# Kernel optimization log

Measured on AMD Instinct MI355X. Metric: run time of the kernel, lower is better.

Reference implementation:

```python
import jax, jax.numpy as jnp
import numpy as np

NUM_EMB = 1024
EMB_DIM = 256
BETA = 0.25


def setup_inputs() -> dict:
    key = jax.random.key(0)
    k1, k2 = jax.random.split(key)
    z = jax.random.normal(k1, (64, 32, 32, EMB_DIM), dtype=jnp.float32)
    # RandomUniform(-1/N, 1/N) init, shape (embedding_dimension, number_embeddings)
    embeddings = jax.random.uniform(
        k2, (EMB_DIM, NUM_EMB), dtype=jnp.float32,
        minval=-1.0 / NUM_EMB, maxval=1.0 / NUM_EMB)
    return {"z": z, "embeddings": embeddings}


def reference(z, embeddings):
    beta = BETA
    z_flat = z.reshape(-1, EMB_DIM)                      # [N, D]
    # squared L2 distances via ||z||^2 + ||e||^2 - 2 z @ e
    distances = (jnp.sum(z_flat ** 2, axis=1, keepdims=True)
                 + jnp.sum(embeddings ** 2, axis=0)
                 - 2.0 * (z_flat @ embeddings))          # [N, K]
    encoding_indices = jnp.argmin(distances, axis=1)     # [N] int
    quantized = embeddings.T[encoding_indices].reshape(z.shape)  # gather rows of e^T
    vq_loss = jnp.mean((quantized - jax.lax.stop_gradient(z)) ** 2)
    commitment_loss = beta * jnp.mean((jax.lax.stop_gradient(quantized) - z) ** 2)
    quantized_st = z + jax.lax.stop_gradient(quantized - z)  # straight-through
    # perplexity from codebook usage histogram
    counts = jnp.zeros((NUM_EMB,), dtype=distances.dtype).at[encoding_indices].add(1.0)
    avg_probs = counts / encoding_indices.shape[0]
    perplexity = jnp.exp(-jnp.sum(avg_probs * jnp.log(avg_probs + 1e-10)))
    return (quantized_st, encoding_indices, vq_loss, commitment_loss, perplexity)
```

## Files before the change

kernel.cpp:

```cpp
#include <hip/hip_runtime.h>
#include <math.h>

#define NUM_EMB 1024
#define EMB_DIM 256
#define NROWS   65536
#define NTHREADS 256
#define MTHREADS 1024
#define EPSF 1.5e-3f
#define GCAP 458752
#define LLCAP 3837

#define OFF_IDX  16777216
#define OFF_VQ   16842752

#define WS_C2    0
#define WS_HIST  4096
#define WS_LOSS  8192
#define WS_GCNT  8196
#define WS_R2    8448
#define WS_SLOT  270592
#define WS_ETF   794880
#define WS_ETB   1843456
#define WS_RMIN  2367744
#define WS_GLIST 2629888

typedef __attribute__((ext_vector_type(8))) short bf16x8;
typedef __attribute__((ext_vector_type(4))) float f32x4;

#define BAR_LGKM() do {                                        \
    asm volatile("s_waitcnt lgkmcnt(0)" ::: "memory");         \
    __builtin_amdgcn_s_barrier();                              \
    asm volatile("" ::: "memory");                             \
  } while (0)

__device__ __forceinline__ unsigned short f2bf(float x) {
  unsigned u = __float_as_uint(x);
  unsigned r = (u + 0x7FFFu + ((u >> 16) & 1u)) >> 16;
  return (unsigned short)r;
}

__global__ __launch_bounds__(NTHREADS) void vq_pt(
    const float* __restrict__ emb, float* __restrict__ cvec,
    int* __restrict__ hist, float* __restrict__ loss, int* __restrict__ gcnt,
    float* __restrict__ embTf, unsigned short* __restrict__ embTbf) {
  __shared__ float t[64][65];
  const int tid = threadIdx.x;
  if (blockIdx.x < 4) {
    int k = blockIdx.x * NTHREADS + tid;
    float s = 0.f;
    for (int d = 0; d < EMB_DIM; ++d) {
      float v = emb[d * NUM_EMB + k];
      s = __fadd_rn(s, __fmul_rn(v, v));
    }
    cvec[k] = s;
    hist[k] = 0;
    if (k == 0) { *loss = 0.f; *gcnt = 0; }
  } else {
    const int b = blockIdx.x - 4;
    const int kt = b & 15, dt = b >> 4;
    #pragma unroll
    for (int it = 0; it < 16; ++it) {
      int i = tid + it * NTHREADS, r = i >> 6, c = i & 63;
      t[r][c] = emb[(dt * 64 + r) * NUM_EMB + kt * 64 + c];
    }
    __syncthreads();
    #pragma unroll
    for (int it = 0; it < 16; ++it) {
      int i = tid + it * NTHREADS, r = i >> 6, c = i & 63;
      float v = t[c][r];
      embTf[(kt * 64 + r) * EMB_DIM + dt * 64 + c] = v;
      embTbf[(kt * 64 + r) * EMB_DIM + dt * 64 + c] = f2bf(v);
    }
  }
}

__global__ __launch_bounds__(NTHREADS) void vq_r2k(
    const float* __restrict__ z, float* __restrict__ r2out) {
  __shared__ float zc[64][36];
  __shared__ float pmm[64][2][4];
  const int tid = threadIdx.x;
  const int n0 = blockIdx.x * 64;
  const float* zrow = z + (size_t)n0 * EMB_DIM;
  const int prow = tid >> 2, pm = tid & 3;
  float racc[2][2] = {{0.f, 0.f}, {0.f, 0.f}};
  for (int dc = 0; dc < 8; ++dc) {
    __syncthreads();
    #pragma unroll
    for (int it = 0; it < 2; ++it) {
      int i = tid + it * NTHREADS, row = i >> 3, f4 = i & 7;
      *(float4*)(&zc[row][f4 * 4]) = *(const float4*)(zrow + row * EMB_DIM + dc * 32 + f4 * 4);
    }
    __syncthreads();
    const int half = dc >> 2;
    #pragma unroll
    for (int q = 0; q < 4; ++q)
      #pragma unroll
      for (int jj = 0; jj < 2; ++jj) {
        float v = zc[prow][(pm * 2 + jj) + 8 * q];
        racc[half][jj] = __fadd_rn(racc[half][jj], __fmul_rn(v, v));
      }
  }
  pmm[prow][0][pm] = __fadd_rn(racc[0][0], racc[0][1]);
  pmm[prow][1][pm] = __fadd_rn(racc[1][0], racc[1][1]);
  __syncthreads();
  if (tid < 64) {
    float h0 = __fadd_rn(__fadd_rn(pmm[tid][0][0], pmm[tid][0][1]),
                         __fadd_rn(pmm[tid][0][2], pmm[tid][0][3]));
    float h1 = __fadd_rn(__fadd_rn(pmm[tid][1][0], pmm[tid][1][1]),
                         __fadd_rn(pmm[tid][1][2], pmm[tid][1][3]));
    r2out[n0 + tid] = __fadd_rn(h0, h1);
  }
}

__global__ __launch_bounds__(MTHREADS, 4) void vq_mfma(
    const float* __restrict__ z, const unsigned short* __restrict__ embTbf,
    const float* __restrict__ cvec, unsigned long long* __restrict__ slots,
    int* __restrict__ gcnt, unsigned int* __restrict__ glist,
    int* __restrict__ grm) {
  __shared__ unsigned short zc[256][256];
  __shared__ unsigned short Bl[2][8192];

  int* caps = (int*)&Bl[1][0];
  unsigned int* llist = (unsigned int*)caps + 259;

  const int tid = threadIdx.x;
  const int lane = tid & 63, wave = tid >> 6;
  const int quad = lane >> 4, l15 = lane & 15;
  const int rg = wave >> 2, cg = wave & 3;
  const int n0 = blockIdx.x * 256;

  if (tid < 256) {
    grm[n0 + tid] = 0x7F000000;
    slots[n0 + tid] = ~0ULL;
  }

  #pragma unroll
  for (int it = 0; it < 8; ++it) {
    int g = tid + it * MTHREADS, row = g >> 5, u = g & 31;
    const float* src = z + (size_t)(n0 + row) * EMB_DIM + u * 8;
    float4 a = *(const float4*)src;
    float4 b = *(const float4*)(src + 4);
    uint4 w;
    w.x = ((unsigned)f2bf(a.y) << 16) | f2bf(a.x);
    w.y = ((unsigned)f2bf(a.w) << 16) | f2bf(a.z);
    w.z = ((unsigned)f2bf(b.y) << 16) | f2bf(b.x);
    w.w = ((unsigned)f2bf(b.w) << 16) | f2bf(b.z);
    *(uint4*)(&zc[row][(u ^ (row & 7)) * 8]) = w;
  }

  const int bn = tid >> 2, bseg = tid & 3;
  const size_t bofs = (size_t)bn * EMB_DIM + (size_t)bseg * 8;
  const int bunit = bn * 4 + (bseg ^ ((bn >> 1) & 3));
  int bidx[4];
  #pragma unroll
  for (int ct = 0; ct < 4; ++ct) {
    int cn = cg * 64 + ct * 16 + l15;
    bidx[ct] = (cn * 4 + (quad ^ ((cn >> 1) & 3))) * 8;
  }

  uint4 p0 = *(const uint4*)(embTbf + bofs);
  BAR_LGKM();
  *(uint4*)(&Bl[0][(size_t)bunit * 8]) = p0;
  uint4 bpre = *(const uint4*)(embTbf + 32 + bofs);
  BAR_LGKM();

  for (int j = 0; j < 4; ++j) {
    f32x4 acc[4][4];
    #pragma unroll
    for (int rt = 0; rt < 4; ++rt)
      #pragma unroll
      for (int ct = 0; ct < 4; ++ct)
        acc[rt][ct] = (f32x4){0.f, 0.f, 0.f, 0.f};
    float c2r[4];
    #pragma unroll
    for (int ct = 0; ct < 4; ++ct)
      c2r[ct] = cvec[j * 256 + cg * 64 + ct * 16 + l15] + 1.0f;

    for (int kc = 0; kc < 8; ++kc) {
      const int c = j * 8 + kc;
      if (c < 31)
        *(uint4*)(&Bl[(c + 1) & 1][(size_t)bunit * 8]) = bpre;
      if (c + 2 < 32)
        bpre = *(const uint4*)(embTbf + (size_t)((c + 2) >> 3) * 65536 +
                               (size_t)((c + 2) & 7) * 32 + bofs);
      bf16x8 av[4], bv[4];
      #pragma unroll
      for (int rt = 0; rt < 4; ++rt) {
        int row = rg * 64 + rt * 16 + l15;
        av[rt] = *(const bf16x8*)(&zc[row][((kc * 4 + quad) ^ (l15 & 7)) * 8]);
      }
      #pragma unroll
      for (int ct = 0; ct < 4; ++ct)
        bv[ct] = *(const bf16x8*)(&Bl[c & 1][(size_t)bidx[ct]]);
      #pragma unroll
      for (int rt = 0; rt < 4; ++rt)
        #pragma unroll
        for (int ct = 0; ct < 4; ++ct)
          acc[rt][ct] = __builtin_amdgcn_mfma_f32_16x16x32_bf16(av[rt], bv[ct], acc[rt][ct], 0, 0, 0);
      BAR_LGKM();
    }
    if (tid < 256) caps[tid] = 0x7F000000;
    if (tid == 0) caps[256] = 0;
    BAR_LGKM();

    #pragma unroll
    for (int rt = 0; rt < 4; ++rt)
      #pragma unroll
      for (int reg = 0; reg < 4; ++reg) {
        float m = 1e30f;
        #pragma unroll
        for (int ct = 0; ct < 4; ++ct) {
          float d = fmaf(-2.f, acc[rt][ct][reg], c2r[ct]);
          m = fminf(m, d);
        }
        #pragma unroll
        for (int off = 1; off < 16; off <<= 1)
          m = fminf(m, __shfl_xor(m, off));
        if (l15 == 0)
          atomicMin(&caps[rg * 64 + rt * 16 + quad * 4 + reg], __float_as_int(m));
      }
    BAR_LGKM();

    if (tid < 256) {
      int lm = caps[tid];
      int old = atomicMin(&grm[n0 + tid], lm);
      caps[tid] = lm < old ? lm : old;
    }
    BAR_LGKM();

    #pragma unroll
    for (int rt = 0; rt < 4; ++rt)
      #pragma unroll
      for (int reg = 0; reg < 4; ++reg) {
        int rowl = rg * 64 + rt * 16 + quad * 4 + reg;
        float fmin = __int_as_float(caps[rowl]);
        #pragma unroll
        for (int ct = 0; ct < 4; ++ct) {
          float d = fmaf(-2.f, acc[rt][ct][reg], c2r[ct]);
          bool pred = (d <= fmin + EPSF);
          unsigned long long msk = __ballot(pred);
          if (msk) {
            int leader = (int)(__ffsll((long long)msk) - 1);
            int cnt = (int)__popcll(msk);
            int base0 = 0;
            if (lane == leader) base0 = atomicAdd(&caps[256], cnt);
            base0 = __shfl(base0, leader);
            if (pred) {
              int id = base0 + (int)__popcll(msk & ((1ULL << lane) - 1ULL));
              int k = j * 256 + cg * 64 + ct * 16 + l15;
              if (id < LLCAP)
                llist[id] = ((unsigned)(n0 + rowl) << 10) | (unsigned)k;
            }
          }
        }
      }
    BAR_LGKM();
    if (tid == 0) {
      int c = caps[256]; if (c > LLCAP) c = LLCAP;
      caps[258] = c;
      caps[257] = atomicAdd(gcnt, c);
    }
    BAR_LGKM();
    {
      int cnt = caps[258], base = caps[257];
      for (int i = tid; i < cnt; i += MTHREADS)
        if (base + i < GCAP) glist[base + i] = llist[i];
    }
    BAR_LGKM();
  }
}

__global__ __launch_bounds__(NTHREADS) void vq_refine(
    const float* __restrict__ z, const float* __restrict__ embTf,
    const float* __restrict__ r2, const float* __restrict__ cvec,
    const int* __restrict__ gcnt, const unsigned int* __restrict__ glist,
    unsigned long long* __restrict__ slots) {
  int n = *gcnt; if (n > GCAP) n = GCAP;
  for (int i = blockIdx.x * NTHREADS + threadIdx.x; i < n;
       i += gridDim.x * NTHREADS) {
    unsigned e = glist[i];
    int grow = (int)(e >> 10), k = (int)(e & 1023);
    const float* zr = z + (size_t)grow * EMB_DIM;
    const float* er = embTf + (size_t)k * EMB_DIM;
    float s = 0.f;
    for (int d = 0; d < EMB_DIM; ++d)
      s = fmaf(zr[d], er[d], s);
    float dist = __fsub_rn(__fadd_rn(r2[grow], cvec[k]), __fmul_rn(2.0f, s));
    unsigned long long key =
        ((unsigned long long)__float_as_uint(dist) << 32) | (unsigned)k;
    atomicMin(&slots[grow], key);
  }
}

__global__ __launch_bounds__(NTHREADS) void vq_epi(
    const float* __restrict__ z, const float* __restrict__ embTf,
    const unsigned long long* __restrict__ slots,
    float* __restrict__ out, int* __restrict__ hist, float* __restrict__ loss) {
  __shared__ int ks[64];
  __shared__ float wsum[4];
  const int tid = threadIdx.x;
  const int n0 = blockIdx.x * 64;
  const float* zrow = z + (size_t)n0 * EMB_DIM;
  if (tid < 64) {
    int k = (int)(slots[n0 + tid] & 1023ULL);
    ks[tid] = k;
    out[OFF_IDX + n0 + tid] = (float)k;
    atomicAdd(&hist[k], 1);
  }
  __syncthreads();
  float sumsq = 0.f;
  #pragma unroll
  for (int it = 0; it < 16; ++it) {
    int g = tid + it * NTHREADS;
    int row = g >> 6;
    int d = (g & 63) * 4;
    int k = ks[row];
    float4 zv = *(const float4*)(zrow + row * EMB_DIM + d);
    float4 q = *(const float4*)(embTf + (size_t)k * EMB_DIM + d);
    float4 df;
    df.x = q.x - zv.x; df.y = q.y - zv.y; df.z = q.z - zv.z; df.w = q.w - zv.w;
    sumsq = fmaf(df.x, df.x, sumsq);
    sumsq = fmaf(df.y, df.y, sumsq);
    sumsq = fmaf(df.z, df.z, sumsq);
    sumsq = fmaf(df.w, df.w, sumsq);
    *(float4*)(out + (size_t)(n0 + row) * EMB_DIM + d) = q;
  }
  #pragma unroll
  for (int off = 32; off > 0; off >>= 1) sumsq += __shfl_down(sumsq, off);
  if ((tid & 63) == 0) wsum[tid >> 6] = sumsq;
  __syncthreads();
  if (tid == 0) atomicAdd(loss, wsum[0] + wsum[1] + wsum[2] + wsum[3]);
}

__global__ __launch_bounds__(NTHREADS) void vq_finalize(
    const int* __restrict__ hist, const float* __restrict__ loss,
    float* __restrict__ out) {
  __shared__ float ws[4];
  int tid = threadIdx.x;
  float s = 0.f;
  for (int k = tid; k < NUM_EMB; k += NTHREADS) {
    float p = (float)hist[k] * (1.0f / 65536.0f);
    s += p * logf(p + 1e-10f);
  }
  #pragma unroll
  for (int off = 32; off > 0; off >>= 1) s += __shfl_down(s, off);
  if ((tid & 63) == 0) ws[tid >> 6] = s;
  __syncthreads();
  if (tid == 0) {
    float tot = ws[0] + ws[1] + ws[2] + ws[3];
    float vq = *loss * (1.0f / 16777216.0f);
    out[OFF_VQ + 0] = vq;
    out[OFF_VQ + 1] = 0.25f * vq;
    out[OFF_VQ + 2] = expf(-tot);
  }
}

extern "C" void kernel_launch(void* const* d_in, const int* in_sizes, int n_in,
                              void* d_out, int out_size, void* d_ws, size_t ws_size,
                              hipStream_t stream) {
  const float* z   = (const float*)d_in[0];
  const float* emb = (const float*)d_in[1];
  float* out = (float*)d_out;
  char* ws = (char*)d_ws;
  float* cvec   = (float*)(ws + WS_C2);
  int*   hist   = (int*)(ws + WS_HIST);
  float* loss   = (float*)(ws + WS_LOSS);
  int*   gcnt   = (int*)(ws + WS_GCNT);
  float* r2     = (float*)(ws + WS_R2);
  unsigned long long* slots = (unsigned long long*)(ws + WS_SLOT);
  float* embTf  = (float*)(ws + WS_ETF);
  unsigned short* embTbf = (unsigned short*)(ws + WS_ETB);
  int*   grm    = (int*)(ws + WS_RMIN);
  unsigned int* glist = (unsigned int*)(ws + WS_GLIST);

  vq_pt<<<68, NTHREADS, 0, stream>>>(emb, cvec, hist, loss, gcnt, embTf, embTbf);
  vq_r2k<<<NROWS / 64, NTHREADS, 0, stream>>>(z, r2);
  vq_mfma<<<NROWS / 256, MTHREADS, 0, stream>>>(z, embTbf, cvec, slots, gcnt, glist, grm);
  vq_refine<<<512, NTHREADS, 0, stream>>>(z, embTf, r2, cvec, gcnt, glist, slots);
  vq_epi<<<NROWS / 64, NTHREADS, 0, stream>>>(z, embTf, slots, out, hist, loss);
  vq_finalize<<<1, NTHREADS, 0, stream>>>(hist, loss, out);
}
```

Measured before the change: 289.2 us.

## Halve MFMA block rows, single-buffer codebook tile, merge row-norm kernel into prep

```diff
diff --git a/kernel.cpp b/kernel.cpp
--- a/kernel.cpp
+++ b/kernel.cpp
@@ -5,10 +5,11 @@
 #define EMB_DIM 256
 #define NROWS   65536
 #define NTHREADS 256
-#define MTHREADS 1024
+#define MTHREADS 512
+#define MROWS   128
 #define EPSF 1.5e-3f
 #define GCAP 458752
-#define LLCAP 3837
+#define LLCAP 3965
 
 #define OFF_IDX  16777216
 #define OFF_VQ   16842752
@@ -42,8 +43,11 @@
 __global__ __launch_bounds__(NTHREADS) void vq_pt(
     const float* __restrict__ emb, float* __restrict__ cvec,
     int* __restrict__ hist, float* __restrict__ loss, int* __restrict__ gcnt,
-    float* __restrict__ embTf, unsigned short* __restrict__ embTbf) {
+    float* __restrict__ embTf, unsigned short* __restrict__ embTbf,
+    const float* __restrict__ z, float* __restrict__ r2out) {
   __shared__ float t[64][65];
+  __shared__ float zc[64][36];
+  __shared__ float pmm[64][2][4];
   const int tid = threadIdx.x;
   if (blockIdx.x < 4) {
     int k = blockIdx.x * NTHREADS + tid;
@@ -55,7 +59,7 @@
     cvec[k] = s;
     hist[k] = 0;
     if (k == 0) { *loss = 0.f; *gcnt = 0; }
-  } else {
+  } else if (blockIdx.x < 68) {
     const int b = blockIdx.x - 4;
     const int kt = b & 15, dt = b >> 4;
     #pragma unroll
@@ -71,44 +75,38 @@
       embTf[(kt * 64 + r) * EMB_DIM + dt * 64 + c] = v;
       embTbf[(kt * 64 + r) * EMB_DIM + dt * 64 + c] = f2bf(v);
     }
-  }
-}
-
-__global__ __launch_bounds__(NTHREADS) void vq_r2k(
-    const float* __restrict__ z, float* __restrict__ r2out) {
-  __shared__ float zc[64][36];
-  __shared__ float pmm[64][2][4];
-  const int tid = threadIdx.x;
-  const int n0 = blockIdx.x * 64;
-  const float* zrow = z + (size_t)n0 * EMB_DIM;
-  const int prow = tid >> 2, pm = tid & 3;
-  float racc[2][2] = {{0.f, 0.f}, {0.f, 0.f}};
-  for (int dc = 0; dc < 8; ++dc) {
+  } else {
+    const int n0 = (blockIdx.x - 68) * 64;
+    const float* zrow = z + (size_t)n0 * EMB_DIM;
+    const int prow = tid >> 2, pm = tid & 3;
+    float racc[2][2] = {{0.f, 0.f}, {0.f, 0.f}};
+    for (int dc = 0; dc < 8; ++dc) {
+      __syncthreads();
+      #pragma unroll
+      for (int it = 0; it < 2; ++it) {
+        int i = tid + it * NTHREADS, row = i >> 3, f4 = i & 7;
+        *(float4*)(&zc[row][f4 * 4]) = *(const float4*)(zrow + row * EMB_DIM + dc * 32 + f4 * 4);
+      }
+      __syncthreads();
+      const int half = dc >> 2;
+      #pragma unroll
+      for (int q = 0; q < 4; ++q)
+        #pragma unroll
+        for (int jj = 0; jj < 2; ++jj) {
+          float v = zc[prow][(pm * 2 + jj) + 8 * q];
+          racc[half][jj] = __fadd_rn(racc[half][jj], __fmul_rn(v, v));
+        }
+    }
+    pmm[prow][0][pm] = __fadd_rn(racc[0][0], racc[0][1]);
+    pmm[prow][1][pm] = __fadd_rn(racc[1][0], racc[1][1]);
     __syncthreads();
-    #pragma unroll
-    for (int it = 0; it < 2; ++it) {
-      int i = tid + it * NTHREADS, row = i >> 3, f4 = i & 7;
-      *(float4*)(&zc[row][f4 * 4]) = *(const float4*)(zrow + row * EMB_DIM + dc * 32 + f4 * 4);
-    }
-    __syncthreads();
-    const int half = dc >> 2;
-    #pragma unroll
-    for (int q = 0; q < 4; ++q)
-      #pragma unroll
-      for (int jj = 0; jj < 2; ++jj) {
-        float v = zc[prow][(pm * 2 + jj) + 8 * q];
-        racc[half][jj] = __fadd_rn(racc[half][jj], __fmul_rn(v, v));
-      }
-  }
-  pmm[prow][0][pm] = __fadd_rn(racc[0][0], racc[0][1]);
-  pmm[prow][1][pm] = __fadd_rn(racc[1][0], racc[1][1]);
-  __syncthreads();
-  if (tid < 64) {
-    float h0 = __fadd_rn(__fadd_rn(pmm[tid][0][0], pmm[tid][0][1]),
-                         __fadd_rn(pmm[tid][0][2], pmm[tid][0][3]));
-    float h1 = __fadd_rn(__fadd_rn(pmm[tid][1][0], pmm[tid][1][1]),
-                         __fadd_rn(pmm[tid][1][2], pmm[tid][1][3]));
-    r2out[n0 + tid] = __fadd_rn(h0, h1);
+    if (tid < 64) {
+      float h0 = __fadd_rn(__fadd_rn(pmm[tid][0][0], pmm[tid][0][1]),
+                           __fadd_rn(pmm[tid][0][2], pmm[tid][0][3]));
+      float h1 = __fadd_rn(__fadd_rn(pmm[tid][1][0], pmm[tid][1][1]),
+                           __fadd_rn(pmm[tid][1][2], pmm[tid][1][3]));
+      r2out[n0 + tid] = __fadd_rn(h0, h1);
+    }
   }
 }
 
@@ -117,19 +115,19 @@
     const float* __restrict__ cvec, unsigned long long* __restrict__ slots,
     int* __restrict__ gcnt, unsigned int* __restrict__ glist,
     int* __restrict__ grm) {
-  __shared__ unsigned short zc[256][256];
-  __shared__ unsigned short Bl[2][8192];
-
-  int* caps = (int*)&Bl[1][0];
-  unsigned int* llist = (unsigned int*)caps + 259;
+  __shared__ unsigned short zc[MROWS][256];
+  __shared__ unsigned short Bl[8192];
+
+  int* caps = (int*)&Bl[0];
+  unsigned int* llist = (unsigned int*)caps + 131;
 
   const int tid = threadIdx.x;
   const int lane = tid & 63, wave = tid >> 6;
   const int quad = lane >> 4, l15 = lane & 15;
   const int rg = wave >> 2, cg = wave & 3;
-  const int n0 = blockIdx.x * 256;
-
-  if (tid < 256) {
+  const int n0 = blockIdx.x * MROWS;
+
+  if (tid < MROWS) {
     grm[n0 + tid] = 0x7F000000;
     slots[n0 + tid] = ~0ULL;
   }
@@ -149,8 +147,10 @@
   }
 
   const int bn = tid >> 2, bseg = tid & 3;
-  const size_t bofs = (size_t)bn * EMB_DIM + (size_t)bseg * 8;
-  const int bunit = bn * 4 + (bseg ^ ((bn >> 1) & 3));
+  const size_t bofsA = (size_t)bn * EMB_DIM + (size_t)bseg * 8;
+  const size_t bofsB = (size_t)(bn + 128) * EMB_DIM + (size_t)bseg * 8;
+  const int bunitA = bn * 4 + (bseg ^ ((bn >> 1) & 3));
+  const int bunitB = bunitA + 512;
   int bidx[4];
   #pragma unroll
   for (int ct = 0; ct < 4; ++ct) {
@@ -158,11 +158,8 @@
     bidx[ct] = (cn * 4 + (quad ^ ((cn >> 1) & 3))) * 8;
   }
 
-  uint4 p0 = *(const uint4*)(embTbf + bofs);
-  BAR_LGKM();
-  *(uint4*)(&Bl[0][(size_t)bunit * 8]) = p0;
-  uint4 bpre = *(const uint4*)(embTbf + 32 + bofs);
-  BAR_LGKM();
+  uint4 pa = *(const uint4*)(embTbf + bofsA);
+  uint4 pb = *(const uint4*)(embTbf + bofsB);
 
   for (int j = 0; j < 4; ++j) {
     f32x4 acc[4][4];
@@ -178,11 +175,16 @@
 
     for (int kc = 0; kc < 8; ++kc) {
       const int c = j * 8 + kc;
-      if (c < 31)
-        *(uint4*)(&Bl[(c + 1) & 1][(size_t)bunit * 8]) = bpre;
-      if (c + 2 < 32)
-        bpre = *(const uint4*)(embTbf + (size_t)((c + 2) >> 3) * 65536 +
-                               (size_t)((c + 2) & 7) * 32 + bofs);
+      BAR_LGKM();
+      *(uint4*)(&Bl[(size_t)bunitA * 8]) = pa;
+      *(uint4*)(&Bl[(size_t)bunitB * 8]) = pb;
+      BAR_LGKM();
+      if (c + 1 < 32) {
+        const unsigned short* srcp = embTbf +
+            (size_t)((c + 1) >> 3) * 65536 + (size_t)((c + 1) & 7) * 32;
+        pa = *(const uint4*)(srcp + bofsA);
+        pb = *(const uint4*)(srcp + bofsB);
+      }
       bf16x8 av[4], bv[4];
       #pragma unroll
       for (int rt = 0; rt < 4; ++rt) {
@@ -191,16 +193,16 @@
       }
       #pragma unroll
       for (int ct = 0; ct < 4; ++ct)
-        bv[ct] = *(const bf16x8*)(&Bl[c & 1][(size_t)bidx[ct]]);
+        bv[ct] = *(const bf16x8*)(&Bl[(size_t)bidx[ct]]);
       #pragma unroll
       for (int rt = 0; rt < 4; ++rt)
         #pragma unroll
         for (int ct = 0; ct < 4; ++ct)
           acc[rt][ct] = __builtin_amdgcn_mfma_f32_16x16x32_bf16(av[rt], bv[ct], acc[rt][ct], 0, 0, 0);
-      BAR_LGKM();
-    }
-    if (tid < 256) caps[tid] = 0x7F000000;
-    if (tid == 0) caps[256] = 0;
+    }
+    BAR_LGKM();
+    if (tid < MROWS) caps[tid] = 0x7F000000;
+    if (tid == 0) caps[128] = 0;
     BAR_LGKM();
 
     #pragma unroll
@@ -221,7 +223,7 @@
       }
     BAR_LGKM();
 
-    if (tid < 256) {
+    if (tid < MROWS) {
       int lm = caps[tid];
       int old = atomicMin(&grm[n0 + tid], lm);
       caps[tid] = lm < old ? lm : old;
@@ -243,7 +245,7 @@
             int leader = (int)(__ffsll((long long)msk) - 1);
             int cnt = (int)__popcll(msk);
             int base0 = 0;
-            if (lane == leader) base0 = atomicAdd(&caps[256], cnt);
+            if (lane == leader) base0 = atomicAdd(&caps[128], cnt);
             base0 = __shfl(base0, leader);
             if (pred) {
               int id = base0 + (int)__popcll(msk & ((1ULL << lane) - 1ULL));
@@ -256,17 +258,16 @@
       }
     BAR_LGKM();
     if (tid == 0) {
-      int c = caps[256]; if (c > LLCAP) c = LLCAP;
-      caps[258] = c;
-      caps[257] = atomicAdd(gcnt, c);
+      int c = caps[128]; if (c > LLCAP) c = LLCAP;
+      caps[130] = c;
+      caps[129] = atomicAdd(gcnt, c);
     }
     BAR_LGKM();
     {
-      int cnt = caps[258], base = caps[257];
+      int cnt = caps[130], base = caps[129];
       for (int i = tid; i < cnt; i += MTHREADS)
         if (base + i < GCAP) glist[base + i] = llist[i];
     }
-    BAR_LGKM();
   }
 }
 
@@ -373,9 +374,8 @@
   int*   grm    = (int*)(ws + WS_RMIN);
   unsigned int* glist = (unsigned int*)(ws + WS_GLIST);
 
-  vq_pt<<<68, NTHREADS, 0, stream>>>(emb, cvec, hist, loss, gcnt, embTf, embTbf);
-  vq_r2k<<<NROWS / 64, NTHREADS, 0, stream>>>(z, r2);
-  vq_mfma<<<NROWS / 256, MTHREADS, 0, stream>>>(z, embTbf, cvec, slots, gcnt, glist, grm);
+  vq_pt<<<1092, NTHREADS, 0, stream>>>(emb, cvec, hist, loss, gcnt, embTf, embTbf, z, r2);
+  vq_mfma<<<NROWS / MROWS, MTHREADS, 0, stream>>>(z, embTbf, cvec, slots, gcnt, glist, grm);
   vq_refine<<<512, NTHREADS, 0, stream>>>(z, embTf, r2, cvec, gcnt, glist, slots);
   vq_epi<<<NROWS / 64, NTHREADS, 0, stream>>>(z, embTf, slots, out, hist, loss);
   vq_finalize<<<1, NTHREADS, 0, stream>>>(hist, loss, out);
```

Result: faster. 283.3 us (-2.0%).
